# Kernel optimization log

Hardware: AMD Instinct MI355X
Metric: run time of the kernel (lower is better)

## Reference

```python
import jax, jax.numpy as jnp
import numpy as np

E, D, H, T = 8, 1024, 2048, 2048  # num_expert, d_model, d_hidden, tokens

def setup_inputs() -> dict:
    key = jax.random.key(0)
    ks = jax.random.split(key, 7)
    return {
        "moe_inp": jax.random.normal(ks[0], (T, D), jnp.float32),
        "Wg": jax.random.normal(ks[1], (D, E), jnp.float32) * 0.02,
        "bg": jnp.zeros((E,), jnp.float32),
        "W1": jax.random.normal(ks[2], (E, D, H), jnp.float32) * 0.02,
        "b1": jnp.zeros((E, H), jnp.float32),
        "W2": jax.random.normal(ks[3], (E, H, D), jnp.float32) * 0.02,
        "b2": jnp.zeros((E, D), jnp.float32),
        "top_k": 2,
    }

def reference(moe_inp, Wg, bg, W1, b1, W2, b2, top_k):
    # NaiveGate: linear gate, top-k select, softmax over the selected logits
    logits = moe_inp @ Wg + bg                      # [T, E]
    top_vals, top_idx = jax.lax.top_k(logits, top_k)  # [T, k]
    gate_score = jax.nn.softmax(top_vals, axis=-1)    # [T, k]

    # Exact (no capacity drop) MoE: scan over experts, mask-combine.
    # Equivalent math to scatter -> per-expert FFN -> gather -> bmm(gate_score, ...).
    def body(acc, xs):
        e, w1, bb1, w2, bb2 = xs
        h = jax.nn.gelu(moe_inp @ w1 + bb1)          # [T, H]
        y = h @ w2 + bb2                             # [T, D]
        w = jnp.sum(jnp.where(top_idx == e, gate_score, 0.0), axis=-1)  # [T]
        return acc + w[:, None] * y, None

    init = jnp.zeros_like(moe_inp)
    xs = (jnp.arange(E), W1, b1, W2, b2)
    moe_outp, _ = jax.lax.scan(body, init, xs)
    return moe_outp, top_idx
```

## Files before the change

kernel.cpp:

```cpp
#include <hip/hip_runtime.h>
#include <stdint.h>

#define T_TOK 2048
#define D_DIM 1024
#define H_DIM 2048
#define N_EXP 8
#define MAXS  4608

#define WS_CNT    0
#define WS_BTOK   256
#define WS_BW     (WS_BTOK + N_EXP*2048*4)
#define WS_XG     (WS_BW + N_EXP*2048*4)
#define WS_HBUF   (WS_XG + (size_t)MAXS*1024*2)
#define WS_W1T    (WS_HBUF + (size_t)MAXS*2048*2)
#define WS_W2T    (WS_W1T + (size_t)N_EXP*1024*2048*2)

typedef __bf16 bf16x8 __attribute__((ext_vector_type(8)));
typedef float  f32x4  __attribute__((ext_vector_type(4)));

__device__ __forceinline__ unsigned short f2bf(float f) {
  unsigned int u = __float_as_uint(f);
  u += 0x7fffu + ((u >> 16) & 1u);
  return (unsigned short)(u >> 16);
}

__device__ __forceinline__ float gelu_tanh(float x) {
  float u = 0.7978845608028654f * (x + 0.044715f * x * x * x);
  return 0.5f * x * (1.0f + tanhf(u));
}

__global__ void zero_kernel(float4* __restrict__ out4, int* __restrict__ cnt) {
  int i = blockIdx.x * 256 + threadIdx.x;
  out4[i] = make_float4(0.f, 0.f, 0.f, 0.f);
  if (blockIdx.x == 0 && threadIdx.x < N_EXP) cnt[threadIdx.x] = 0;
}

__global__ void gate_kernel(const float* __restrict__ x, const float* __restrict__ Wg,
                            const float* __restrict__ bg, float* __restrict__ out_idx,
                            int* __restrict__ cnt, int* __restrict__ btok,
                            float* __restrict__ bw) {
  const int lane = threadIdx.x & 63;
  const int t = blockIdx.x * 4 + (threadIdx.x >> 6);
  float p[8];
#pragma unroll
  for (int i = 0; i < 8; ++i) p[i] = 0.f;
  const float* xr = x + (size_t)t * D_DIM;
  for (int i = lane; i < D_DIM; i += 64) {
    const float xv = xr[i];
    const float4 wa = ((const float4*)(Wg + i * 8))[0];
    const float4 wb = ((const float4*)(Wg + i * 8))[1];
    p[0] += xv * wa.x; p[1] += xv * wa.y; p[2] += xv * wa.z; p[3] += xv * wa.w;
    p[4] += xv * wb.x; p[5] += xv * wb.y; p[6] += xv * wb.z; p[7] += xv * wb.w;
  }
#pragma unroll
  for (int off = 32; off > 0; off >>= 1) {
#pragma unroll
    for (int i = 0; i < 8; ++i) p[i] += __shfl_xor(p[i], off);
  }
  if (lane == 0) {
#pragma unroll
    for (int i = 0; i < 8; ++i) p[i] += bg[i];
    int i0 = 0; float v0 = p[0];
#pragma unroll
    for (int i = 1; i < 8; ++i) if (p[i] > v0) { v0 = p[i]; i0 = i; }
    int i1 = -1; float v1 = -3.4e38f;
#pragma unroll
    for (int i = 0; i < 8; ++i) if (i != i0 && p[i] > v1) { v1 = p[i]; i1 = i; }
    const float ex = expf(v1 - v0);
    const float inv = 1.f / (1.f + ex);
    out_idx[t * 2 + 0] = (float)i0;
    out_idx[t * 2 + 1] = (float)i1;
    int s0 = atomicAdd(&cnt[i0], 1);
    btok[i0 * 2048 + s0] = t; bw[i0 * 2048 + s0] = inv;
    int s1 = atomicAdd(&cnt[i1], 1);
    btok[i1 * 2048 + s1] = t; bw[i1 * 2048 + s1] = ex * inv;
  }
}

__global__ void transpose_cvt(const float* __restrict__ W1, unsigned short* __restrict__ W1t,
                              const float* __restrict__ W2, unsigned short* __restrict__ W2t) {
  const int set = blockIdx.z;
  const int e = blockIdx.y;
  const int lin = blockIdx.x;
  const int R = set ? H_DIM : D_DIM;
  const int C = set ? D_DIM : H_DIM;
  const int tx = set ? (lin & 15) : (lin & 31);
  const int ty = set ? (lin >> 4) : (lin >> 5);
  const float* in = (set ? W2 : W1) + (size_t)e * (D_DIM * H_DIM);
  unsigned short* out = (set ? W2t : W1t) + (size_t)e * (D_DIM * H_DIM);
  const int c0 = tx * 64, r0 = ty * 64;
  __shared__ float tile[64][68];
  const int tid = threadIdx.x;
#pragma unroll
  for (int p = 0; p < 4; ++p) {
    const int idx = p * 256 + tid;
    const int r = idx >> 4, c4 = idx & 15;
    *(float4*)&tile[r][c4 * 4] = *(const float4*)(in + (size_t)(r0 + r) * C + c0 + c4 * 4);
  }
  __syncthreads();
#pragma unroll
  for (int p = 0; p < 2; ++p) {
    const int idx = p * 256 + tid;
    const int oc = idx >> 3, seg = idx & 7;
    unsigned u[4];
#pragma unroll
    for (int j = 0; j < 4; ++j) {
      const unsigned lo = f2bf(tile[seg * 8 + 2 * j][oc]);
      const unsigned hi = f2bf(tile[seg * 8 + 2 * j + 1][oc]);
      u[j] = lo | (hi << 16);
    }
    *(uint4*)(out + (size_t)(c0 + oc) * R + r0 + seg * 8) = make_uint4(u[0], u[1], u[2], u[3]);
  }
}

__device__ __forceinline__ void expert_seg(const int* __restrict__ cnt, int e,
                                           int& base, int& ce, int& pcnt, int& total) {
  int off = 0; base = 0; ce = 0; pcnt = 0;
#pragma unroll
  for (int i = 0; i < N_EXP; ++i) {
    const int c = cnt[i];
    const int p = (c + 63) & ~63;
    if (i == e) { base = off; ce = c; pcnt = p; }
    off += p;
  }
  total = off;
}

__global__ void gather_cvt(const float* __restrict__ x, const int* __restrict__ cnt,
                           const int* __restrict__ btok, unsigned short* __restrict__ Xg) {
  const int s = blockIdx.x;
  int off = 0, e = -1, loc = 0, c_e = 0;
#pragma unroll
  for (int i = 0; i < N_EXP; ++i) {
    const int c = cnt[i];
    const int p = (c + 63) & ~63;
    if (e < 0 && s < off + p) { e = i; loc = s - off; c_e = c; }
    off += p;
  }
  if (e < 0) return;
  uint2* orow = (uint2*)(Xg + (size_t)s * D_DIM);
  if (loc < c_e) {
    const int t = btok[e * 2048 + loc];
    const float4 v = ((const float4*)(x + (size_t)t * D_DIM))[threadIdx.x];
    uint2 u;
    u.x = (unsigned)f2bf(v.x) | ((unsigned)f2bf(v.y) << 16);
    u.y = (unsigned)f2bf(v.z) | ((unsigned)f2bf(v.w) << 16);
    orow[threadIdx.x] = u;
  } else {
    orow[threadIdx.x] = make_uint2(0u, 0u);
  }
}

template <int MODE>
__global__ void __launch_bounds__(256) moe_gemm(
    const unsigned short* __restrict__ A, const unsigned short* __restrict__ B,
    const float* __restrict__ bias, const int* __restrict__ cnt,
    const int* __restrict__ btok, const float* __restrict__ bw,
    unsigned short* __restrict__ Hout, float* __restrict__ out) {
  constexpr int K   = (MODE == 0) ? D_DIM : H_DIM;
  constexpr int SK  = (MODE == 0) ? 1 : 2;
  constexpr int KS  = K / SK;
  constexpr int NIT = KS / 32;

  const int lin = blockIdx.x;
  const int glo = lin & 7;
  const int mt  = (lin >> 3) & 31;
  const int g   = ((lin >> 8) << 3) | glo;
  int nt, e, ksl;
  if (MODE == 0) { nt = g & 15; e = g >> 4; ksl = 0; }
  else           { nt = g & 7;  e = (g >> 3) & 7; ksl = g >> 6; }

  int base, ce, pcnt, total;
  expert_seg(cnt, e, base, ce, pcnt, total);
  if (mt * 64 >= pcnt) return;
  const int row0 = base + mt * 64;
  const int n0 = nt * 128;

  __shared__ __align__(16) unsigned short As[2][64 * 32];
  __shared__ __align__(16) unsigned short Bs[2][128 * 32];

  const int tid = threadIdx.x;
  const int lane = tid & 63;
  const int wv = tid >> 6;
  const int wm = wv >> 1;
  const int wn = wv & 1;

  const unsigned short* Ab = A + (size_t)row0 * K + ksl * KS;
  const unsigned short* Bb = B + (size_t)e * ((size_t)H_DIM * D_DIM) + (size_t)n0 * K + ksl * KS;

  f32x4 acc[2][4];
#pragma unroll
  for (int i = 0; i < 2; ++i)
#pragma unroll
    for (int j = 0; j < 4; ++j) acc[i][j] = (f32x4)(0.0f);

  const int subr = lane >> 2;
  const int ks = (lane & 3) * 8;
  const int fr = lane & 15;
  const int kq = (lane >> 4) * 8;

  auto stage = [&](int kt, int b) {
    const int k0 = kt * 32;
    {
      const int r = wv * 16 + subr;
      const unsigned short* ga = Ab + (size_t)r * K + (k0 + ks);
      __builtin_amdgcn_global_load_lds(
          (__attribute__((address_space(1))) void*)ga,
          (__attribute__((address_space(3))) void*)(As[b] + wv * 16 * 32), 16, 0, 0);
    }
#pragma unroll
    for (int it = 0; it < 2; ++it) {
      const int ci = wv + it * 4;
      const int r = ci * 16 + subr;
      const unsigned short* gb = Bb + (size_t)r * K + (k0 + ks);
      __builtin_amdgcn_global_load_lds(
          (__attribute__((address_space(1))) void*)gb,
          (__attribute__((address_space(3))) void*)(Bs[b] + ci * 16 * 32), 16, 0, 0);
    }
  };

  stage(0, 0);
  for (int i = 0; i < NIT; ++i) {
    const int b = i & 1;
    __syncthreads();
    if (i + 1 < NIT) stage(i + 1, b ^ 1);
    bf16x8 av[2], bv[4];
#pragma unroll
    for (int mi = 0; mi < 2; ++mi)
      av[mi] = *(const bf16x8*)(As[b] + (wm * 32 + mi * 16 + fr) * 32 + kq);
#pragma unroll
    for (int ni = 0; ni < 4; ++ni)
      bv[ni] = *(const bf16x8*)(Bs[b] + (wn * 64 + ni * 16 + fr) * 32 + kq);
#pragma unroll
    for (int mi = 0; mi < 2; ++mi)
#pragma unroll
      for (int ni = 0; ni < 4; ++ni)
        acc[mi][ni] = __builtin_amdgcn_mfma_f32_16x16x32_bf16(av[mi], bv[ni], acc[mi][ni], 0, 0, 0);
  }

  if (MODE == 0) {
    const float* bb = bias + (size_t)e * H_DIM + n0;
#pragma unroll
    for (int mi = 0; mi < 2; ++mi) {
      const int rb = wm * 32 + mi * 16 + (lane >> 4) * 4;
#pragma unroll
      for (int r = 0; r < 4; ++r) {
        unsigned short* hp = Hout + (size_t)(row0 + rb + r) * H_DIM + n0;
#pragma unroll
        for (int ni = 0; ni < 4; ++ni) {
          const int col = wn * 64 + ni * 16 + fr;
          hp[col] = f2bf(gelu_tanh(acc[mi][ni][r] + bb[col]));
        }
      }
    }
  } else {
    const float* bb = bias + (size_t)e * D_DIM + n0;
#pragma unroll
    for (int mi = 0; mi < 2; ++mi) {
      const int rb = wm * 32 + mi * 16 + (lane >> 4) * 4;
#pragma unroll
      for (int r = 0; r < 4; ++r) {
        const int local = mt * 64 + rb + r;
        if (local < ce) {
          const int tok = btok[e * 2048 + local];
          const float w = bw[e * 2048 + local];
          float* op = out + (size_t)tok * D_DIM + n0;
#pragma unroll
          for (int ni = 0; ni < 4; ++ni) {
            const int col = wn * 64 + ni * 16 + fr;
            const float bias_once = (ksl == 0) ? bb[col] : 0.f;
            atomicAdd(op + col, w * (acc[mi][ni][r] + bias_once));
          }
        }
      }
    }
  }
}

extern "C" void kernel_launch(void* const* d_in, const int* in_sizes, int n_in,
                              void* d_out, int out_size, void* d_ws, size_t ws_size,
                              hipStream_t stream) {
  const float* moe_inp = (const float*)d_in[0];
  const float* Wg = (const float*)d_in[1];
  const float* bg = (const float*)d_in[2];
  const float* W1 = (const float*)d_in[3];
  const float* b1 = (const float*)d_in[4];
  const float* W2 = (const float*)d_in[5];
  const float* b2 = (const float*)d_in[6];
  float* out = (float*)d_out;

  char* ws = (char*)d_ws;
  int* cnt  = (int*)(ws + WS_CNT);
  int* btok = (int*)(ws + WS_BTOK);
  float* bw = (float*)(ws + WS_BW);
  unsigned short* Xg   = (unsigned short*)(ws + WS_XG);
  unsigned short* Hbuf = (unsigned short*)(ws + WS_HBUF);
  unsigned short* W1t  = (unsigned short*)(ws + WS_W1T);
  unsigned short* W2t  = (unsigned short*)(ws + WS_W2T);

  zero_kernel<<<dim3(2048), dim3(256), 0, stream>>>((float4*)out, cnt);
  gate_kernel<<<dim3(T_TOK / 4), dim3(256), 0, stream>>>(moe_inp, Wg, bg,
                                                         out + (size_t)T_TOK * D_DIM,
                                                         cnt, btok, bw);
  transpose_cvt<<<dim3(512, N_EXP, 2), dim3(256), 0, stream>>>(W1, W1t, W2, W2t);
  gather_cvt<<<dim3(MAXS), dim3(256), 0, stream>>>(moe_inp, cnt, btok, Xg);
  moe_gemm<0><<<dim3(4096), dim3(256), 0, stream>>>(
      Xg, W1t, b1, cnt, btok, bw, Hbuf, nullptr);
  moe_gemm<1><<<dim3(4096), dim3(256), 0, stream>>>(
      Hbuf, W2t, b2, cnt, btok, bw, nullptr, out);
}
```

Baseline: 339.8 us.

## Double K tile to 64 with XOR-style swizzled LDS layout and occupancy hint

Doubles the K-step per pipeline stage from 32 to 64, halving the number of barriers and loop iterations per tile. Shared-memory rows are stored with a rotated 16-byte slot layout so fragment reads avoid bank conflicts, and the global-to-LDS loads are remapped to match. A launch-bounds occupancy hint of 3 blocks per CU is added. The changes double LDS use per block and may constrain register allocation.

```diff
diff --git a/kernel.cpp b/kernel.cpp
--- a/kernel.cpp
+++ b/kernel.cpp
@@ -114,7 +114,7 @@
 }
 
 __device__ __forceinline__ void expert_seg(const int* __restrict__ cnt, int e,
-                                           int& base, int& ce, int& pcnt, int& total) {
+                                           int& base, int& ce, int& pcnt) {
   int off = 0; base = 0; ce = 0; pcnt = 0;
 #pragma unroll
   for (int i = 0; i < N_EXP; ++i) {
@@ -123,7 +123,6 @@
     if (i == e) { base = off; ce = c; pcnt = p; }
     off += p;
   }
-  total = off;
 }
 
 __global__ void gather_cvt(const float* __restrict__ x, const int* __restrict__ cnt,
@@ -152,7 +151,7 @@
 }
 
 template <int MODE>
-__global__ void __launch_bounds__(256) moe_gemm(
+__global__ void __launch_bounds__(256, 3) moe_gemm(
     const unsigned short* __restrict__ A, const unsigned short* __restrict__ B,
     const float* __restrict__ bias, const int* __restrict__ cnt,
     const int* __restrict__ btok, const float* __restrict__ bw,
@@ -160,7 +159,7 @@
   constexpr int K   = (MODE == 0) ? D_DIM : H_DIM;
   constexpr int SK  = (MODE == 0) ? 1 : 2;
   constexpr int KS  = K / SK;
-  constexpr int NIT = KS / 32;
+  constexpr int NIT = KS / 64;
 
   const int lin = blockIdx.x;
   const int glo = lin & 7;
@@ -170,14 +169,14 @@
   if (MODE == 0) { nt = g & 15; e = g >> 4; ksl = 0; }
   else           { nt = g & 7;  e = (g >> 3) & 7; ksl = g >> 6; }
 
-  int base, ce, pcnt, total;
-  expert_seg(cnt, e, base, ce, pcnt, total);
+  int base, ce, pcnt;
+  expert_seg(cnt, e, base, ce, pcnt);
   if (mt * 64 >= pcnt) return;
   const int row0 = base + mt * 64;
   const int n0 = nt * 128;
 
-  __shared__ __align__(16) unsigned short As[2][64 * 32];
-  __shared__ __align__(16) unsigned short Bs[2][128 * 32];
+  __shared__ __align__(16) unsigned short As[2][64 * 64];
+  __shared__ __align__(16) unsigned short Bs[2][128 * 64];
 
   const int tid = threadIdx.x;
   const int lane = tid & 63;
@@ -194,28 +193,31 @@
 #pragma unroll
     for (int j = 0; j < 4; ++j) acc[i][j] = (f32x4)(0.0f);
 
-  const int subr = lane >> 2;
-  const int ks = (lane & 3) * 8;
+  const int rloc = lane >> 3;
+  const int q = lane & 7;
+  const int gq = ((q - rloc) & 7) * 8;
   const int fr = lane & 15;
-  const int kq = (lane >> 4) * 8;
+  const int kg = lane >> 4;
 
   auto stage = [&](int kt, int b) {
-    const int k0 = kt * 32;
-    {
-      const int r = wv * 16 + subr;
-      const unsigned short* ga = Ab + (size_t)r * K + (k0 + ks);
+    const int k0 = kt * 64;
+#pragma unroll
+    for (int it = 0; it < 2; ++it) {
+      const int ci = wv * 2 + it;
+      const int r = ci * 8 + rloc;
+      const unsigned short* ga = Ab + (size_t)r * K + (k0 + gq);
       __builtin_amdgcn_global_load_lds(
           (__attribute__((address_space(1))) void*)ga,
-          (__attribute__((address_space(3))) void*)(As[b] + wv * 16 * 32), 16, 0, 0);
-    }
-#pragma unroll
-    for (int it = 0; it < 2; ++it) {
-      const int ci = wv + it * 4;
-      const int r = ci * 16 + subr;
-      const unsigned short* gb = Bb + (size_t)r * K + (k0 + ks);
+          (__attribute__((address_space(3))) void*)(As[b] + ci * 8 * 64), 16, 0, 0);
+    }
+#pragma unroll
+    for (int it = 0; it < 4; ++it) {
+      const int ci = wv * 4 + it;
+      const int r = ci * 8 + rloc;
+      const unsigned short* gb = Bb + (size_t)r * K + (k0 + gq);
       __builtin_amdgcn_global_load_lds(
           (__attribute__((address_space(1))) void*)gb,
-          (__attribute__((address_space(3))) void*)(Bs[b] + ci * 16 * 32), 16, 0, 0);
+          (__attribute__((address_space(3))) void*)(Bs[b] + ci * 8 * 64), 16, 0, 0);
     }
   };
 
@@ -224,18 +226,30 @@
     const int b = i & 1;
     __syncthreads();
     if (i + 1 < NIT) stage(i + 1, b ^ 1);
-    bf16x8 av[2], bv[4];
-#pragma unroll
-    for (int mi = 0; mi < 2; ++mi)
-      av[mi] = *(const bf16x8*)(As[b] + (wm * 32 + mi * 16 + fr) * 32 + kq);
-#pragma unroll
-    for (int ni = 0; ni < 4; ++ni)
-      bv[ni] = *(const bf16x8*)(Bs[b] + (wn * 64 + ni * 16 + fr) * 32 + kq);
-#pragma unroll
-    for (int mi = 0; mi < 2; ++mi)
-#pragma unroll
-      for (int ni = 0; ni < 4; ++ni)
-        acc[mi][ni] = __builtin_amdgcn_mfma_f32_16x16x32_bf16(av[mi], bv[ni], acc[mi][ni], 0, 0, 0);
+    bf16x8 av[2][2], bv[2][4];
+#pragma unroll
+    for (int kk = 0; kk < 2; ++kk) {
+#pragma unroll
+      for (int mi = 0; mi < 2; ++mi) {
+        const int rr = wm * 32 + mi * 16 + fr;
+        const int slot = ((kk * 4 + kg) + (rr & 7)) & 7;
+        av[kk][mi] = *(const bf16x8*)(As[b] + rr * 64 + slot * 8);
+      }
+#pragma unroll
+      for (int ni = 0; ni < 4; ++ni) {
+        const int rr = wn * 64 + ni * 16 + fr;
+        const int slot = ((kk * 4 + kg) + (rr & 7)) & 7;
+        bv[kk][ni] = *(const bf16x8*)(Bs[b] + rr * 64 + slot * 8);
+      }
+    }
+#pragma unroll
+    for (int kk = 0; kk < 2; ++kk)
+#pragma unroll
+      for (int mi = 0; mi < 2; ++mi)
+#pragma unroll
+        for (int ni = 0; ni < 4; ++ni)
+          acc[mi][ni] = __builtin_amdgcn_mfma_f32_16x16x32_bf16(av[kk][mi], bv[kk][ni],
+                                                                acc[mi][ni], 0, 0, 0);
   }
 
   if (MODE == 0) {
```

Result: no change. 345.7 us (+1.7%).
